# Performance work log

Measured on AMD Instinct MI355X. Metric: run time of the kernel, lower is better.

## Reference

```python
import jax, jax.numpy as jnp
import numpy as np

B, T, N = 16, 2048, 24
K, C_IN, C0, C1 = 3, 1, 64, 64
KS, PRED_LEN = 3, 24
EPS = 1e-5


def _norm_laplacian(adj):
    # L = D^-1/2 A^T D^-1/2 (matches scipy path: (A D^-1/2)^T D^-1/2)
    d = adj.sum(axis=1)
    dis = jnp.where(d > 0, 1.0 / jnp.sqrt(d), 0.0)
    return dis[:, None] * adj.T * dis[None, :]


def _cheb_stack(L, k_terms):
    polys = [jnp.eye(N, dtype=L.dtype), L]
    for _ in range(2, k_terms):
        polys.append(2.0 * L @ polys[-1] - polys[-2])
    return jnp.stack(polys[:k_terms])  # (K, N, N)


def _causal_conv(x, w, b, dilation):
    ks = w.shape[-1]
    pad = (ks - 1) * dilation
    x = jnp.pad(x, ((0, 0), (0, 0), (0, 0), (pad, 0)))
    y = jax.lax.conv_general_dilated(
        x, w, window_strides=(1, 1), padding='VALID',
        rhs_dilation=(1, dilation),
        dimension_numbers=('NCHW', 'OIHW', 'NCHW'))
    return y + b[None, :, None, None]


def _bn(x, g, be):
    # training-mode batch norm over (B, N, T) per channel
    mu = x.mean(axis=(0, 2, 3), keepdims=True)
    var = x.var(axis=(0, 2, 3), keepdims=True)
    return g[None, :, None, None] * (x - mu) * jax.lax.rsqrt(var + EPS) + be[None, :, None, None]


def setup_inputs() -> dict:
    key = jax.random.key(0)
    ks = jax.random.split(key, 16)
    s = 0.05
    return {
        'batch_x': jax.random.normal(ks[0], (B, T, N), jnp.float32),
        'adj': jax.random.uniform(ks[1], (N, N), jnp.float32),
        'theta': jax.random.normal(ks[2], (K, C_IN, C0), jnp.float32),  # Theta per Cheb term
        'w1a': jax.random.normal(ks[3], (C0, C0, 1, KS), jnp.float32) * s,
        'b1a': jnp.zeros((C0,), jnp.float32),
        'g1a': jnp.ones((C0,), jnp.float32), 'be1a': jnp.zeros((C0,), jnp.float32),
        'w1b': jax.random.normal(ks[4], (C0, C0, 1, KS), jnp.float32) * s,
        'b1b': jnp.zeros((C0,), jnp.float32),
        'g1b': jnp.ones((C0,), jnp.float32), 'be1b': jnp.zeros((C0,), jnp.float32),
        'w2a': jax.random.normal(ks[5], (C1, C0, 1, KS), jnp.float32) * s,
        'b2a': jnp.zeros((C1,), jnp.float32),
        'g2a': jnp.ones((C1,), jnp.float32), 'be2a': jnp.zeros((C1,), jnp.float32),
        'w2b': jax.random.normal(ks[6], (C1, C1, 1, KS), jnp.float32) * s,
        'b2b': jnp.zeros((C1,), jnp.float32),
        'g2b': jnp.ones((C1,), jnp.float32), 'be2b': jnp.zeros((C1,), jnp.float32),
        'w_end': jax.random.normal(ks[7], (C1 // 2, C1, 1, 1), jnp.float32) * s,
        'b_end': jnp.zeros((C1 // 2,), jnp.float32),
        'w_end1': jax.random.normal(ks[8], (1, C1 // 2, 1, 2), jnp.float32) * s,
        'b_end1': jnp.zeros((1,), jnp.float32),
    }


def reference(batch_x, adj, theta,
              w1a, b1a, g1a, be1a, w1b, b1b, g1b, be1b,
              w2a, b2a, g2a, be2a, w2b, b2b, g2b, be2b,
              w_end, b_end, w_end1, b_end1):
    # (B, T, N) -> (B, 1, N, T)
    x = jnp.transpose(batch_x, (0, 2, 1))[:, None, :, :]

    # --- Cheb_conv: fused over K terms and all timesteps ---
    L = _norm_laplacian(adj)
    Tk = _cheb_stack(L, K)                       # (K, N, N)
    xp = jnp.transpose(x, (0, 2, 1, 3))          # (B, N, C_in, T)
    # out[b,o,n,t] = sum_{k,m,c} xp[b,m,c,t] Tk[k,m,n] theta[k,c,o]
    gc = jnp.einsum('bmct,kmn,kco->bont', xp, Tk, theta)  # (B, C0, N, T)

    # --- TCN block 1 (dilation 1), residual is identity (C0 == C0) ---
    h = jax.nn.relu(_bn(_causal_conv(gc, w1a, b1a, 1), g1a, be1a))
    h = jax.nn.relu(_bn(_causal_conv(h, w1b, b1b, 1), g1b, be1b))
    out0 = jax.nn.relu(h + gc)

    # --- TCN block 2 (dilation 2), residual identity (C0 == C1), no final relu ---
    h = jax.nn.relu(_bn(_causal_conv(out0, w2a, b2a, 2), g2a, be2a))
    h = jax.nn.relu(_bn(_causal_conv(h, w2b, b2b, 2), g2b, be2b))
    out = h + out0                               # (B, C1, N, T)

    # --- head: 1x1 conv + relu, then (1,2) valid conv -> 1 channel ---
    e = jax.lax.conv_general_dilated(out, w_end, (1, 1), 'VALID',
                                     dimension_numbers=('NCHW', 'OIHW', 'NCHW'))
    e = jax.nn.relu(e + b_end[None, :, None, None])
    e = jax.lax.conv_general_dilated(e, w_end1, (1, 1), 'VALID',
                                     dimension_numbers=('NCHW', 'OIHW', 'NCHW'))
    e = e + b_end1[None, :, None, None]          # (B, 1, N, T-1)
    e = e[:, 0, :, -PRED_LEN:]                   # (B, N, pred_len)
    return jnp.transpose(e, (0, 2, 1))           # (B, pred_len, N)
```

## Files before the change

### kernel.cpp

```cpp
#include <hip/hip_runtime.h>
#include <cmath>

#define TPB 256

typedef __attribute__((ext_vector_type(8)))  short short8;
typedef __attribute__((ext_vector_type(16))) float float16;

static constexpr int  BB   = 16;
static constexpr int  TDIM = 2048;
static constexpr int  NN   = 24;
static constexpr int  P    = BB * NN;
static constexpr int  C    = 64;
static constexpr int  TILE = 256;
static constexpr int  NBT  = TDIM / TILE;
static constexpr int  NSHARD = 64;
static constexpr float INV_CNT = 1.0f / 786432.0f;
static constexpr int  XPITCH = 72;

static constexpr size_t OFF_TK    = 0;
static constexpr size_t OFF_WEFF  = 6912;
static constexpr size_t OFF_WFRAG = 9216;
static constexpr size_t OFF_ST    = 82944;
static constexpr size_t OFF_BNAB  = 214016;
static constexpr size_t OFF_O0    = 216320;
static constexpr size_t OFF_YT    = 2673920;
static constexpr size_t OFF_S     = 5131520;
static constexpr size_t OFF_YA    = 14568704;
static constexpr size_t OFF_YB    = 115232000;

__device__ __forceinline__ unsigned short f2bf(float f) {
    unsigned int i = __float_as_uint(f);
    i += 0x7FFFu + ((i >> 16) & 1u);
    return (unsigned short)(i >> 16);
}
__device__ __forceinline__ float bf2f(unsigned short u) {
    return __uint_as_float((unsigned)u << 16);
}

__global__ __launch_bounds__(TPB)
void prep_kernel(const float* __restrict__ adj, const float* __restrict__ theta,
                 const float* __restrict__ w1a,
                 const float* __restrict__ w1b, const float* __restrict__ w2a,
                 const float* __restrict__ w2b,
                 float* __restrict__ tk, float* __restrict__ weff,
                 unsigned short* __restrict__ wf, float* __restrict__ stats)
{
    const int tid = threadIdx.x;
    if (blockIdx.x < 144) {
        int e = blockIdx.x * TPB + tid;
        int conv = e / 12288, r = e % 12288;
        int oh = r / 6144; r %= 6144;
        int kc = r / 512;  r %= 512;
        int lane = r / 8;
        int jj = r % 8;
        int o = oh * 32 + (lane & 31);
        int K = kc * 16 + (lane >> 5) * 8 + jj;
        int j = K / 64, c2 = K % 64;
        const float* w = (conv == 0) ? w1b : ((conv == 1) ? w2a : w2b);
        wf[e] = f2bf(w[(o * 64 + c2) * 3 + j]);
        return;
    }

    __shared__ float disl[24];
    __shared__ float Ll[576];
    __shared__ float T2l[576];

    for (int e = tid; e < 4 * 2 * 64 * NSHARD; e += TPB) stats[e] = 0.f;

    if (tid < 24) {
        float d = 0.f;
        for (int j = 0; j < 24; ++j) d += adj[tid * 24 + j];
        disl[tid] = (d > 0.f) ? 1.0f / sqrtf(d) : 0.f;
    }
    __syncthreads();
    for (int e = tid; e < 576; e += TPB) {
        int i = e / 24, j = e % 24;
        Ll[e] = disl[i] * adj[j * 24 + i] * disl[j];
    }
    __syncthreads();
    for (int e = tid; e < 576; e += TPB) {
        int i = e / 24, j = e % 24;
        float a = 0.f;
        for (int m = 0; m < 24; ++m) a += Ll[i * 24 + m] * Ll[m * 24 + j];
        T2l[e] = 2.f * a - ((i == j) ? 1.f : 0.f);
    }
    __syncthreads();
    for (int e = tid; e < 576; e += TPB) {
        int i = e / 24, j = e % 24;
        tk[e]        = (i == j) ? 1.f : 0.f;
        tk[576 + e]  = Ll[e];
        tk[1152 + e] = T2l[e];
    }
    for (int e = tid; e < 576; e += TPB) {
        int o = e / 9, k = (e % 9) / 3, j = e % 3;
        float a = 0.f;
        for (int c2 = 0; c2 < 64; ++c2)
            a += w1a[(o * 64 + c2) * 3 + j] * theta[k * 64 + c2];
        weff[(k * 3 + j) * 64 + o] = a;
    }
}

__global__ __launch_bounds__(TPB)
void bnprep_kernel(const float* __restrict__ stats, const float* __restrict__ g,
                   const float* __restrict__ be, float2* __restrict__ ab)
{
    const int tid = threadIdx.x;
    const int ch = tid >> 2, q = tid & 3;
    float s1 = 0.f, s2 = 0.f;
    #pragma unroll
    for (int u = 0; u < 16; ++u) {
        int sh = q * 16 + u;
        s1 += stats[ch * 64 + sh];
        s2 += stats[(64 + ch) * 64 + sh];
    }
    s1 += __shfl_xor(s1, 1); s1 += __shfl_xor(s1, 2);
    s2 += __shfl_xor(s2, 1); s2 += __shfl_xor(s2, 2);
    if (q == 0) {
        float mu  = s1 * INV_CNT;
        float var = s2 * INV_CNT - mu * mu;
        float a = g[ch] * (1.0f / sqrtf(var + 1e-5f));
        ab[ch] = make_float2(a, be[ch] - mu * a);
    }
}

__global__ __launch_bounds__(TPB)
void s_kernel(const float* __restrict__ bx, const float* __restrict__ tk,
              float* __restrict__ sbuf)
{
    __shared__ float bxs[256 * 25];
    __shared__ float tkl[1728];
    const int tid = threadIdx.x;
    const int b  = blockIdx.x >> 3;
    const int t0 = (blockIdx.x & 7) * 256;

    for (int e = tid; e < 1728; e += TPB) tkl[e] = tk[e];
    for (int e = tid; e < 256 * 24; e += TPB) {
        int t = e / 24, m = e % 24;
        bxs[t * 25 + m] = bx[((long)b * TDIM + t0 + t) * NN + m];
    }
    __syncthreads();

    const int t = tid;
    for (int k = 0; k < 3; ++k) {
        float acc[24];
        #pragma unroll
        for (int n = 0; n < 24; ++n) acc[n] = 0.f;
        for (int m = 0; m < 24; ++m) {
            float xb = bxs[t * 25 + m];
            const float* tr = tkl + k * 576 + m * 24;
            #pragma unroll
            for (int n = 0; n < 24; ++n) acc[n] = fmaf(xb, tr[n], acc[n]);
        }
        for (int n = 0; n < 24; ++n)
            sbuf[((long)k * P + b * NN + n) * TDIM + t0 + t] = acc[n];
    }
}

__global__ __launch_bounds__(TPB)
void stats1a_kernel(const float* __restrict__ sbuf, const float* __restrict__ weff,
                    float* __restrict__ statsOut)
{
    __shared__ float4 ssl4[3 * 66];
    __shared__ float4 wl4[144];
    __shared__ float  part[4][2][64];
    const int tid = threadIdx.x;
    const int blk = blockIdx.x;
    const int p  = blk >> 3;
    const int t0 = (blk & 7) * TILE;

    for (int e = tid; e < 576; e += TPB) ((float*)wl4)[e] = weff[e];
    for (int e = tid; e < 3 * 65; e += TPB) {
        int k = e / 65, u4 = e % 65;
        int t = t0 - 4 + u4 * 4;
        float4 v = make_float4(0.f, 0.f, 0.f, 0.f);
        if (t >= 0) v = *(const float4*)(sbuf + ((long)k * P + p) * TDIM + t);
        ssl4[k * 66 + u4] = v;
    }
    __syncthreads();

    const int oq = tid & 7;
    const int tq = tid >> 3;
    float acc[8][8];
    #pragma unroll
    for (int i = 0; i < 8; ++i)
        #pragma unroll
        for (int ti = 0; ti < 8; ++ti) acc[i][ti] = 0.f;

    #pragma unroll
    for (int k = 0; k < 3; ++k) {
        float4 x0 = ssl4[k * 66 + tq * 2];
        float4 x1 = ssl4[k * 66 + tq * 2 + 1];
        float4 x2 = ssl4[k * 66 + tq * 2 + 2];
        float xv[12] = { x0.x,x0.y,x0.z,x0.w, x1.x,x1.y,x1.z,x1.w, x2.x,x2.y,x2.z,x2.w };
        #pragma unroll
        for (int j = 0; j < 3; ++j) {
            float4 w0 = wl4[(k * 3 + j) * 16 + oq * 2];
            float4 w1 = wl4[(k * 3 + j) * 16 + oq * 2 + 1];
            float wv[8] = { w0.x,w0.y,w0.z,w0.w, w1.x,w1.y,w1.z,w1.w };
            #pragma unroll
            for (int i = 0; i < 8; ++i)
                #pragma unroll
                for (int ti = 0; ti < 8; ++ti)
                    acc[i][ti] = fmaf(wv[i], xv[ti + 2 + j], acc[i][ti]);
        }
    }

    float s1v[8], s2v[8];
    #pragma unroll
    for (int i = 0; i < 8; ++i) {
        float a1 = 0.f, a2 = 0.f;
        #pragma unroll
        for (int ti = 0; ti < 8; ++ti) { a1 += acc[i][ti]; a2 += acc[i][ti] * acc[i][ti]; }
        s1v[i] = a1; s2v[i] = a2;
    }
    #pragma unroll
    for (int m = 8; m < 64; m <<= 1) {
        #pragma unroll
        for (int i = 0; i < 8; ++i) {
            s1v[i] += __shfl_xor(s1v[i], m);
            s2v[i] += __shfl_xor(s2v[i], m);
        }
    }
    const int wave = tid >> 6, lane = tid & 63;
    if (lane < 8) {
        #pragma unroll
        for (int i = 0; i < 8; ++i) {
            part[wave][0][oq * 8 + i] = s1v[i];
            part[wave][1][oq * 8 + i] = s2v[i];
        }
    }
    __syncthreads();
    if (tid < 128) {
        int s = tid >> 6, o = tid & 63;
        float tot = part[0][s][o] + part[1][s][o] + part[2][s][o] + part[3][s][o];
        atomicAdd(&statsOut[(s * 64 + o) * NSHARD + (blk & 63)], tot);
    }
}

template<int MODE>
__global__ __launch_bounds__(TPB)
void conv_mfma(const float* __restrict__ sbuf, const unsigned short* __restrict__ yin,
               unsigned short* __restrict__ yout, float* __restrict__ ytail,
               const unsigned short* __restrict__ wf, const float* __restrict__ weff,
               const float2* __restrict__ bnab, float* __restrict__ statsOut,
               const float* __restrict__ theta, float* __restrict__ o0s)
{
    __shared__ unsigned short Xl[260 * XPITCH];
    __shared__ float4 ssl4[3 * 66];
    __shared__ float  weffl[576];
    __shared__ float  thl[192];
    __shared__ float2 abl[64];
    __shared__ float  parts[4][8][8][2];

    const int tid  = threadIdx.x;
    const int lane = tid & 63;
    const int w    = tid >> 6;
    const int oh   = w & 1;
    const int l31  = lane & 31;
    const int h    = lane >> 5;
    const int blk  = blockIdx.x;
    const int p    = blk >> 3;
    const int tile = blk & 7;
    const int t0   = tile * TILE;
    const float* sslf = (const float*)ssl4;

    short8 af[12];
    #pragma unroll
    for (int kc = 0; kc < 12; ++kc)
        af[kc] = *((const short8*)wf + (oh * 12 + kc) * 64 + lane);

    if (tid < 64) abl[tid] = bnab[tid];
    if (MODE == 0)
        for (int e = tid; e < 576; e += TPB) weffl[e] = weff[e];
    if (MODE == 1)
        for (int e = tid; e < 192; e += TPB) thl[e] = theta[e];
    if (MODE <= 1) {
        for (int e = tid; e < 3 * 66; e += TPB) {
            int k = e / 66, u4 = e % 66;
            int t = t0 - 8 + u4 * 4;
            float4 v = make_float4(0.f, 0.f, 0.f, 0.f);
            if (t >= 0) v = *(const float4*)(sbuf + ((long)k * P + p) * TDIM + t);
            ssl4[k * 66 + u4] = v;
        }
    }
    __syncthreads();

    for (int e = tid; e < 260 * 8; e += TPB) {
        const int tt = e >> 3, cb = e & 7;
        const int t = t0 - 4 + tt;
        float xv[8];
        if (t < 0) {
            #pragma unroll
            for (int r = 0; r < 8; ++r) xv[r] = 0.f;
        } else if (MODE == 0) {
            float sv[9];
            #pragma unroll
            for (int k = 0; k < 3; ++k)
                #pragma unroll
                for (int j = 0; j < 3; ++j)
                    sv[k * 3 + j] = sslf[k * 264 + tt + 2 + j];
            #pragma unroll
            for (int r = 0; r < 8; ++r) {
                int c = cb * 8 + r;
                float raw = 0.f;
                #pragma unroll
                for (int q = 0; q < 9; ++q)
                    raw = fmaf(weffl[q * 64 + c], sv[q], raw);
                float2 ab = abl[c];
                xv[r] = fmaxf(fmaf(ab.x, raw, ab.y), 0.f);
            }
        } else {
            short8 yv8 = *(const short8*)(yin + ((long)p * TDIM + t) * 64 + cb * 8);
            float gcb[3];
            if (MODE == 1) {
                gcb[0] = sslf[      tt + 4];
                gcb[1] = sslf[264 + tt + 4];
                gcb[2] = sslf[528 + tt + 4];
            }
            #pragma unroll
            for (int r = 0; r < 8; ++r) {
                int c = cb * 8 + r;
                float2 ab = abl[c];
                float v = bf2f((unsigned short)yv8[r]);
                float hh = fmaxf(fmaf(ab.x, v, ab.y), 0.f);
                if (MODE == 1) {
                    float gc = thl[c] * gcb[0] + thl[64 + c] * gcb[1] + thl[128 + c] * gcb[2];
                    hh = fmaxf(hh + gc, 0.f);
                }
                xv[r] = hh;
            }
        }
        if (MODE == 1 && tile == 7 && tt >= 235) {
            #pragma unroll
            for (int r = 0; r < 8; ++r)
                o0s[(long)p * 1600 + (cb * 8 + r) * 25 + (tt - 235)] = xv[r];
        }
        short8 pk;
        #pragma unroll
        for (int r = 0; r < 8; ++r) pk[r] = (short)f2bf(xv[r]);
        *(short8*)(Xl + tt * XPITCH + cb * 8) = pk;
    }
    __syncthreads();

    float16 acc[4];
    #pragma unroll
    for (int i = 0; i < 4; ++i)
        #pragma unroll
        for (int r = 0; r < 16; ++r) acc[i][r] = 0.f;

    const int tqb = (w >> 1) * 4;
    #pragma unroll
    for (int kc = 0; kc < 12; ++kc) {
        const int j = kc >> 2;
        const int roff = (MODE == 0) ? (2 + j) : (2 * j);
        const int cbase = (kc & 3) * 16 + h * 8;
        #pragma unroll
        for (int i = 0; i < 4; ++i) {
            int row = (tqb + i) * 32 + l31 + roff;
            short8 bfr = *(const short8*)(Xl + row * XPITCH + cbase);
            acc[i] = __builtin_amdgcn_mfma_f32_32x32x16_bf16(af[kc], bfr, acc[i], 0, 0, 0);
        }
    }

    __syncthreads();

    if (MODE == 2 && tile == 7) {
        #pragma unroll
        for (int i = 0; i < 4; ++i) {
            int tg = t0 + (tqb + i) * 32 + l31;
            if (tg >= TDIM - 25) {
                #pragma unroll
                for (int r = 0; r < 16; ++r) {
                    int o = oh * 32 + (r & 3) + 8 * (r >> 2) + 4 * h;
                    ytail[((long)p * C + o) * 25 + (tg - (TDIM - 25))] = acc[i][r];
                }
            }
        }
    }

    #pragma unroll
    for (int i = 0; i < 4; ++i) {
        int tl = (tqb + i) * 32 + l31;
        #pragma unroll
        for (int q = 0; q < 4; ++q) {
            int ob = oh * 32 + 8 * q + 4 * h;
            ushort4 pk;
            pk.x = f2bf(acc[i][4 * q + 0]);
            pk.y = f2bf(acc[i][4 * q + 1]);
            pk.z = f2bf(acc[i][4 * q + 2]);
            pk.w = f2bf(acc[i][4 * q + 3]);
            *(ushort4*)(Xl + tl * XPITCH + ob) = pk;
        }
    }
    __syncthreads();

    const int cb = tid & 7;
    float s1[8], s2[8];
    #pragma unroll
    for (int r = 0; r < 8; ++r) { s1[r] = 0.f; s2[r] = 0.f; }
    for (int e = tid; e < 2048; e += TPB) {
        int tt = e >> 3;
        short8 v = *(const short8*)(Xl + tt * XPITCH + cb * 8);
        if (MODE <= 1)
            *(short8*)(yout + ((long)p * TDIM + t0 + tt) * 64 + cb * 8) = v;
        #pragma unroll
        for (int r = 0; r < 8; ++r) {
            float f = bf2f((unsigned short)v[r]);
            s1[r] += f;
            s2[r] = fmaf(f, f, s2[r]);
        }
    }
    #pragma unroll
    for (int m = 8; m <= 32; m <<= 1) {
        #pragma unroll
        for (int r = 0; r < 8; ++r) {
            s1[r] += __shfl_xor(s1[r], m);
            s2[r] += __shfl_xor(s2[r], m);
        }
    }
    if (lane < 8) {
        #pragma unroll
        for (int r = 0; r < 8; ++r) {
            parts[w][lane][r][0] = s1[r];
            parts[w][lane][r][1] = s2[r];
        }
    }
    __syncthreads();
    if (tid < 64) {
        int o = tid, cbo = o >> 3, r = o & 7;
        float t1 = parts[0][cbo][r][0] + parts[1][cbo][r][0]
                 + parts[2][cbo][r][0] + parts[3][cbo][r][0];
        float t2 = parts[0][cbo][r][1] + parts[1][cbo][r][1]
                 + parts[2][cbo][r][1] + parts[3][cbo][r][1];
        atomicAdd(&statsOut[o * NSHARD + (blk & 63)], t1);
        atomicAdd(&statsOut[(64 + o) * NSHARD + (blk & 63)], t2);
    }
}

__global__ __launch_bounds__(TPB)
void end_kernel(const float* __restrict__ ytail, const float* __restrict__ o0s,
                const float2* __restrict__ bnab, const float* __restrict__ w_end,
                const float* __restrict__ b_end, const float* __restrict__ w_end1,
                const float* __restrict__ b_end1, float* __restrict__ out)
{
    __shared__ float2 abl[64];
    __shared__ float outl[64 * 25];
    __shared__ float e1l[32 * 25];
    __shared__ float wendl[2048];
    const int tid = threadIdx.x;
    const int p = blockIdx.x;
    const int b = p / 24, n = p % 24;

    if (tid < 64) abl[tid] = bnab[tid];
    for (int e = tid; e < 2048; e += TPB) wendl[e] = w_end[e];
    __syncthreads();

    for (int e = tid; e < 1600; e += TPB) {
        int c = e / 25, tau = e % 25;
        float v = ytail[((long)p * C + c) * 25 + tau];
        float2 ab = abl[c];
        outl[e] = fmaxf(ab.x * v + ab.y, 0.f) + o0s[(long)p * 1600 + e];
    }
    __syncthreads();
    for (int e = tid; e < 800; e += TPB) {
        int q = e / 25, tau = e % 25;
        float a = b_end[q];
        for (int c = 0; c < 64; ++c)
            a = fmaf(wendl[q * 64 + c], outl[c * 25 + tau], a);
        e1l[e] = fmaxf(a, 0.f);
    }
    __syncthreads();
    if (tid < 24) {
        float a = b_end1[0];
        #pragma unroll
        for (int q = 0; q < 32; ++q)
            a += w_end1[q * 2] * e1l[q * 25 + tid] + w_end1[q * 2 + 1] * e1l[q * 25 + tid + 1];
        out[((long)b * 24 + tid) * 24 + n] = a;
    }
}

extern "C" void kernel_launch(void* const* d_in, const int* in_sizes, int n_in,
                              void* d_out, int out_size, void* d_ws, size_t ws_size,
                              hipStream_t stream)
{
    (void)in_sizes; (void)n_in; (void)out_size; (void)ws_size;
    const float* bx    = (const float*)d_in[0];
    const float* adj   = (const float*)d_in[1];
    const float* theta = (const float*)d_in[2];
    const float* w1a   = (const float*)d_in[3];
    const float* g1a   = (const float*)d_in[5];
    const float* be1a  = (const float*)d_in[6];
    const float* w1b   = (const float*)d_in[7];
    const float* g1b   = (const float*)d_in[9];
    const float* be1b  = (const float*)d_in[10];
    const float* w2a   = (const float*)d_in[11];
    const float* g2a   = (const float*)d_in[13];
    const float* be2a  = (const float*)d_in[14];
    const float* w2b   = (const float*)d_in[15];
    const float* g2b   = (const float*)d_in[17];
    const float* be2b  = (const float*)d_in[18];
    const float* wend  = (const float*)d_in[19];
    const float* bend  = (const float*)d_in[20];
    const float* wend1 = (const float*)d_in[21];
    const float* bend1 = (const float*)d_in[22];

    char* ws = (char*)d_ws;
    float*          tk    = (float*)(ws + OFF_TK);
    float*          weff  = (float*)(ws + OFF_WEFF);
    unsigned short* wf    = (unsigned short*)(ws + OFF_WFRAG);
    float*          stats = (float*)(ws + OFF_ST);
    float2*         bnab  = (float2*)(ws + OFF_BNAB);
    float*          o0s   = (float*)(ws + OFF_O0);
    float*          ytail = (float*)(ws + OFF_YT);
    float*          sb    = (float*)(ws + OFF_S);
    unsigned short* yA    = (unsigned short*)(ws + OFF_YA);
    unsigned short* yB    = (unsigned short*)(ws + OFF_YB);

    prep_kernel   <<<145, TPB, 0, stream>>>(adj, theta, w1a, w1b, w2a, w2b,
                                            tk, weff, wf, stats);
    s_kernel      <<<128, TPB, 0, stream>>>(bx, tk, sb);
    stats1a_kernel<<<P * NBT, TPB, 0, stream>>>(sb, weff, stats);
    bnprep_kernel <<<1, TPB, 0, stream>>>(stats,         g1a, be1a, bnab);

    conv_mfma<0><<<P * NBT, TPB, 0, stream>>>(
        sb, nullptr, yA, nullptr, wf, weff,
        bnab, stats + 8192, nullptr, nullptr);
    bnprep_kernel <<<1, TPB, 0, stream>>>(stats + 8192,  g1b, be1b, bnab + 64);

    conv_mfma<1><<<P * NBT, TPB, 0, stream>>>(
        sb, yA, yB, nullptr, wf + 12288, nullptr,
        bnab + 64, stats + 16384, theta, o0s);
    bnprep_kernel <<<1, TPB, 0, stream>>>(stats + 16384, g2a, be2a, bnab + 128);

    conv_mfma<2><<<P * NBT, TPB, 0, stream>>>(
        sb, yB, nullptr, ytail, wf + 24576, nullptr,
        bnab + 128, stats + 24576, nullptr, nullptr);
    bnprep_kernel <<<1, TPB, 0, stream>>>(stats + 24576, g2b, be2b, bnab + 192);

    end_kernel<<<P, TPB, 0, stream>>>(ytail, o0s, bnab + 192,
                                      wend, bend, wend1, bend1, (float*)d_out);
}
```

Before: 359.5 us.

## Fold BN-prep into consumer kernels and halve conv time tile

Removes the four single-block bnprep launches by having each conv block and the end kernel compute the batch-norm scale/shift from the stats shards at startup. The conv_mfma time tile drops from 256 to 128, doubling the grid to 6144 blocks with half the LDS and accumulators per block, for better occupancy and load balance. In exchange, every block redundantly reads 32 KB of stats, and halo loads make up a larger share of each smaller tile.

```diff
diff --git a/kernel.cpp b/kernel.cpp
--- a/kernel.cpp
+++ b/kernel.cpp
@@ -11,17 +11,17 @@
 static constexpr int  NN   = 24;
 static constexpr int  P    = BB * NN;
 static constexpr int  C    = 64;
-static constexpr int  TILE = 256;
-static constexpr int  NBT  = TDIM / TILE;
+static constexpr int  CTILE = 128;
+static constexpr int  CNBT  = TDIM / CTILE;
 static constexpr int  NSHARD = 64;
 static constexpr float INV_CNT = 1.0f / 786432.0f;
 static constexpr int  XPITCH = 72;
+static constexpr int  SPITCH = 136;
 
 static constexpr size_t OFF_TK    = 0;
 static constexpr size_t OFF_WEFF  = 6912;
 static constexpr size_t OFF_WFRAG = 9216;
 static constexpr size_t OFF_ST    = 82944;
-static constexpr size_t OFF_BNAB  = 214016;
 static constexpr size_t OFF_O0    = 216320;
 static constexpr size_t OFF_YT    = 2673920;
 static constexpr size_t OFF_S     = 5131520;
@@ -35,6 +35,29 @@
 }
 __device__ __forceinline__ float bf2f(unsigned short u) {
     return __uint_as_float((unsigned)u << 16);
+}
+
+__device__ __forceinline__
+void bn_from_stats(const float* __restrict__ statsIn, const float* __restrict__ g,
+                   const float* __restrict__ be, float2* abl, int tid)
+{
+    const int ch = tid >> 2, q = tid & 3;
+    float s1 = 0.f, s2 = 0.f;
+    #pragma unroll
+    for (int u = 0; u < 4; ++u) {
+        float4 a = *(const float4*)(statsIn + tid * 16 + u * 4);
+        float4 b = *(const float4*)(statsIn + 4096 + tid * 16 + u * 4);
+        s1 += a.x + a.y + a.z + a.w;
+        s2 += b.x + b.y + b.z + b.w;
+    }
+    s1 += __shfl_xor(s1, 1); s1 += __shfl_xor(s1, 2);
+    s2 += __shfl_xor(s2, 1); s2 += __shfl_xor(s2, 2);
+    if (q == 0) {
+        float mu  = s1 * INV_CNT;
+        float var = s2 * INV_CNT - mu * mu;
+        float a = g[ch] * (1.0f / sqrtf(var + 1e-5f));
+        abl[ch] = make_float2(a, be[ch] - mu * a);
+    }
 }
 
 __global__ __launch_bounds__(TPB)
@@ -65,7 +88,7 @@
     __shared__ float Ll[576];
     __shared__ float T2l[576];
 
-    for (int e = tid; e < 4 * 2 * 64 * NSHARD; e += TPB) stats[e] = 0.f;
+    for (int e = tid; e < 4 * 8192; e += TPB) stats[e] = 0.f;
 
     if (tid < 24) {
         float d = 0.f;
@@ -101,29 +124,6 @@
 }
 
 __global__ __launch_bounds__(TPB)
-void bnprep_kernel(const float* __restrict__ stats, const float* __restrict__ g,
-                   const float* __restrict__ be, float2* __restrict__ ab)
-{
-    const int tid = threadIdx.x;
-    const int ch = tid >> 2, q = tid & 3;
-    float s1 = 0.f, s2 = 0.f;
-    #pragma unroll
-    for (int u = 0; u < 16; ++u) {
-        int sh = q * 16 + u;
-        s1 += stats[ch * 64 + sh];
-        s2 += stats[(64 + ch) * 64 + sh];
-    }
-    s1 += __shfl_xor(s1, 1); s1 += __shfl_xor(s1, 2);
-    s2 += __shfl_xor(s2, 1); s2 += __shfl_xor(s2, 2);
-    if (q == 0) {
-        float mu  = s1 * INV_CNT;
-        float var = s2 * INV_CNT - mu * mu;
-        float a = g[ch] * (1.0f / sqrtf(var + 1e-5f));
-        ab[ch] = make_float2(a, be[ch] - mu * a);
-    }
-}
-
-__global__ __launch_bounds__(TPB)
 void s_kernel(const float* __restrict__ bx, const float* __restrict__ tk,
               float* __restrict__ sbuf)
 {
@@ -166,7 +166,7 @@
     const int tid = threadIdx.x;
     const int blk = blockIdx.x;
     const int p  = blk >> 3;
-    const int t0 = (blk & 7) * TILE;
+    const int t0 = (blk & 7) * 256;
 
     for (int e = tid; e < 576; e += TPB) ((float*)wl4)[e] = weff[e];
     for (int e = tid; e < 3 * 65; e += TPB) {
@@ -242,11 +242,12 @@
 void conv_mfma(const float* __restrict__ sbuf, const unsigned short* __restrict__ yin,
                unsigned short* __restrict__ yout, float* __restrict__ ytail,
                const unsigned short* __restrict__ wf, const float* __restrict__ weff,
-               const float2* __restrict__ bnab, float* __restrict__ statsOut,
+               const float* __restrict__ statsIn, const float* __restrict__ g,
+               const float* __restrict__ be, float* __restrict__ statsOut,
                const float* __restrict__ theta, float* __restrict__ o0s)
 {
-    __shared__ unsigned short Xl[260 * XPITCH];
-    __shared__ float4 ssl4[3 * 66];
+    __shared__ unsigned short Xl[132 * XPITCH];
+    __shared__ float  ssl[3 * SPITCH];
     __shared__ float  weffl[576];
     __shared__ float  thl[192];
     __shared__ float2 abl[64];
@@ -256,36 +257,39 @@
     const int lane = tid & 63;
     const int w    = tid >> 6;
     const int oh   = w & 1;
+    const int th   = w >> 1;
     const int l31  = lane & 31;
     const int h    = lane >> 5;
     const int blk  = blockIdx.x;
-    const int p    = blk >> 3;
-    const int tile = blk & 7;
-    const int t0   = tile * TILE;
-    const float* sslf = (const float*)ssl4;
+    const int p    = blk >> 4;
+    const int tile = blk & 15;
+    const int t0   = tile * CTILE;
 
     short8 af[12];
     #pragma unroll
     for (int kc = 0; kc < 12; ++kc)
         af[kc] = *((const short8*)wf + (oh * 12 + kc) * 64 + lane);
 
-    if (tid < 64) abl[tid] = bnab[tid];
+    bn_from_stats(statsIn, g, be, abl, tid);
+
     if (MODE == 0)
         for (int e = tid; e < 576; e += TPB) weffl[e] = weff[e];
     if (MODE == 1)
         for (int e = tid; e < 192; e += TPB) thl[e] = theta[e];
     if (MODE <= 1) {
-        for (int e = tid; e < 3 * 66; e += TPB) {
-            int k = e / 66, u4 = e % 66;
+        for (int e = tid; e < 3 * 34; e += TPB) {
+            int k = e / 34, u4 = e % 34;
             int t = t0 - 8 + u4 * 4;
             float4 v = make_float4(0.f, 0.f, 0.f, 0.f);
             if (t >= 0) v = *(const float4*)(sbuf + ((long)k * P + p) * TDIM + t);
-            ssl4[k * 66 + u4] = v;
-        }
-    }
-    __syncthreads();
-
-    for (int e = tid; e < 260 * 8; e += TPB) {
+            *(float4*)(ssl + k * SPITCH + u4 * 4) = v;
+        }
+    }
+    __syncthreads();
+
+    const unsigned short* yinb = (MODE >= 1)
+        ? (yin + ((long)p * TDIM + t0 - 4) * 64) : nullptr;
+    for (int e = tid; e < 132 * 8; e += TPB) {
         const int tt = e >> 3, cb = e & 7;
         const int t = t0 - 4 + tt;
         float xv[8];
@@ -298,7 +302,7 @@
             for (int k = 0; k < 3; ++k)
                 #pragma unroll
                 for (int j = 0; j < 3; ++j)
-                    sv[k * 3 + j] = sslf[k * 264 + tt + 2 + j];
+                    sv[k * 3 + j] = ssl[k * SPITCH + tt + 2 + j];
             #pragma unroll
             for (int r = 0; r < 8; ++r) {
                 int c = cb * 8 + r;
@@ -310,12 +314,12 @@
                 xv[r] = fmaxf(fmaf(ab.x, raw, ab.y), 0.f);
             }
         } else {
-            short8 yv8 = *(const short8*)(yin + ((long)p * TDIM + t) * 64 + cb * 8);
+            short8 yv8 = *(const short8*)(yinb + (long)e * 8);
             float gcb[3];
             if (MODE == 1) {
-                gcb[0] = sslf[      tt + 4];
-                gcb[1] = sslf[264 + tt + 4];
-                gcb[2] = sslf[528 + tt + 4];
+                gcb[0] = ssl[              tt + 4];
+                gcb[1] = ssl[SPITCH     + tt + 4];
+                gcb[2] = ssl[2 * SPITCH + tt + 4];
             }
             #pragma unroll
             for (int r = 0; r < 8; ++r) {
@@ -330,10 +334,10 @@
                 xv[r] = hh;
             }
         }
-        if (MODE == 1 && tile == 7 && tt >= 235) {
+        if (MODE == 1 && tile == 15 && tt >= 107) {
             #pragma unroll
             for (int r = 0; r < 8; ++r)
-                o0s[(long)p * 1600 + (cb * 8 + r) * 25 + (tt - 235)] = xv[r];
+                o0s[(long)p * 1600 + (cb * 8 + r) * 25 + (tt - 107)] = xv[r];
         }
         short8 pk;
         #pragma unroll
@@ -342,32 +346,31 @@
     }
     __syncthreads();
 
-    float16 acc[4];
-    #pragma unroll
-    for (int i = 0; i < 4; ++i)
+    float16 acc[2];
+    #pragma unroll
+    for (int i = 0; i < 2; ++i)
         #pragma unroll
         for (int r = 0; r < 16; ++r) acc[i][r] = 0.f;
 
-    const int tqb = (w >> 1) * 4;
+    const unsigned short* xb = Xl + (th * 64 + l31) * XPITCH + h * 8;
     #pragma unroll
     for (int kc = 0; kc < 12; ++kc) {
         const int j = kc >> 2;
         const int roff = (MODE == 0) ? (2 + j) : (2 * j);
-        const int cbase = (kc & 3) * 16 + h * 8;
-        #pragma unroll
-        for (int i = 0; i < 4; ++i) {
-            int row = (tqb + i) * 32 + l31 + roff;
-            short8 bfr = *(const short8*)(Xl + row * XPITCH + cbase);
+        const int coff = (kc & 3) * 16;
+        #pragma unroll
+        for (int i = 0; i < 2; ++i) {
+            short8 bfr = *(const short8*)(xb + (i * 32 + roff) * XPITCH + coff);
             acc[i] = __builtin_amdgcn_mfma_f32_32x32x16_bf16(af[kc], bfr, acc[i], 0, 0, 0);
         }
     }
 
     __syncthreads();
 
-    if (MODE == 2 && tile == 7) {
-        #pragma unroll
-        for (int i = 0; i < 4; ++i) {
-            int tg = t0 + (tqb + i) * 32 + l31;
+    if (MODE == 2 && tile == 15) {
+        #pragma unroll
+        for (int i = 0; i < 2; ++i) {
+            int tg = t0 + (th * 2 + i) * 32 + l31;
             if (tg >= TDIM - 25) {
                 #pragma unroll
                 for (int r = 0; r < 16; ++r) {
@@ -379,8 +382,8 @@
     }
 
     #pragma unroll
-    for (int i = 0; i < 4; ++i) {
-        int tl = (tqb + i) * 32 + l31;
+    for (int i = 0; i < 2; ++i) {
+        int tl = (th * 2 + i) * 32 + l31;
         #pragma unroll
         for (int q = 0; q < 4; ++q) {
             int ob = oh * 32 + 8 * q + 4 * h;
@@ -395,14 +398,16 @@
     __syncthreads();
 
     const int cb = tid & 7;
+    unsigned short* youtb = (MODE <= 1)
+        ? (yout + ((long)p * TDIM + t0) * 64) : nullptr;
     float s1[8], s2[8];
     #pragma unroll
     for (int r = 0; r < 8; ++r) { s1[r] = 0.f; s2[r] = 0.f; }
-    for (int e = tid; e < 2048; e += TPB) {
+    for (int e = tid; e < 1024; e += TPB) {
         int tt = e >> 3;
         short8 v = *(const short8*)(Xl + tt * XPITCH + cb * 8);
         if (MODE <= 1)
-            *(short8*)(yout + ((long)p * TDIM + t0 + tt) * 64 + cb * 8) = v;
+            *(short8*)(youtb + (long)e * 8) = v;
         #pragma unroll
         for (int r = 0; r < 8; ++r) {
             float f = bf2f((unsigned short)v[r]);
@@ -439,7 +444,8 @@
 
 __global__ __launch_bounds__(TPB)
 void end_kernel(const float* __restrict__ ytail, const float* __restrict__ o0s,
-                const float2* __restrict__ bnab, const float* __restrict__ w_end,
+                const float* __restrict__ statsIn, const float* __restrict__ g,
+                const float* __restrict__ be, const float* __restrict__ w_end,
                 const float* __restrict__ b_end, const float* __restrict__ w_end1,
                 const float* __restrict__ b_end1, float* __restrict__ out)
 {
@@ -451,7 +457,7 @@
     const int p = blockIdx.x;
     const int b = p / 24, n = p % 24;
 
-    if (tid < 64) abl[tid] = bnab[tid];
+    bn_from_stats(statsIn, g, be, abl, tid);
     for (int e = tid; e < 2048; e += TPB) wendl[e] = w_end[e];
     __syncthreads();
 
@@ -509,7 +515,6 @@
     float*          weff  = (float*)(ws + OFF_WEFF);
     unsigned short* wf    = (unsigned short*)(ws + OFF_WFRAG);
     float*          stats = (float*)(ws + OFF_ST);
-    float2*         bnab  = (float2*)(ws + OFF_BNAB);
     float*          o0s   = (float*)(ws + OFF_O0);
     float*          ytail = (float*)(ws + OFF_YT);
     float*          sb    = (float*)(ws + OFF_S);
@@ -519,24 +524,18 @@
     prep_kernel   <<<145, TPB, 0, stream>>>(adj, theta, w1a, w1b, w2a, w2b,
                                             tk, weff, wf, stats);
     s_kernel      <<<128, TPB, 0, stream>>>(bx, tk, sb);
-    stats1a_kernel<<<P * NBT, TPB, 0, stream>>>(sb, weff, stats);
-    bnprep_kernel <<<1, TPB, 0, stream>>>(stats,         g1a, be1a, bnab);
-
-    conv_mfma<0><<<P * NBT, TPB, 0, stream>>>(
+    stats1a_kernel<<<P * 8, TPB, 0, stream>>>(sb, weff, stats);
+
+    conv_mfma<0><<<P * CNBT, TPB, 0, stream>>>(
         sb, nullptr, yA, nullptr, wf, weff,
-        bnab, stats + 8192, nullptr, nullptr);
-    bnprep_kernel <<<1, TPB, 0, stream>>>(stats + 8192,  g1b, be1b, bnab + 64);
-
-    conv_mfma<1><<<P * NBT, TPB, 0, stream>>>(
+        stats, g1a, be1a, stats + 8192, nullptr, nullptr);
+    conv_mfma<1><<<P * CNBT, TPB, 0, stream>>>(
         sb, yA, yB, nullptr, wf + 12288, nullptr,
-        bnab + 64, stats + 16384, theta, o0s);
-    bnprep_kernel <<<1, TPB, 0, stream>>>(stats + 16384, g2a, be2a, bnab + 128);
-
-    conv_mfma<2><<<P * NBT, TPB, 0, stream>>>(
+        stats + 8192, g1b, be1b, stats + 16384, theta, o0s);
+    conv_mfma<2><<<P * CNBT, TPB, 0, stream>>>(
         sb, yB, nullptr, ytail, wf + 24576, nullptr,
-        bnab + 128, stats + 24576, nullptr, nullptr);
-    bnprep_kernel <<<1, TPB, 0, stream>>>(stats + 24576, g2b, be2b, bnab + 192);
-
-    end_kernel<<<P, TPB, 0, stream>>>(ytail, o0s, bnab + 192,
+        stats + 16384, g2a, be2a, stats + 24576, nullptr, nullptr);
+
+    end_kernel<<<P, TPB, 0, stream>>>(ytail, o0s, stats + 24576, g2b, be2b,
                                       wend, bend, wend1, bend1, (float*)d_out);
 }
```

Result: slower. 397.6 us (+10.6%).
